# Kernel tuning notes

Hardware: AMD Instinct MI355X
Metric: run time of the kernel (lower is better)

The kernel has to match this reference:

```python
import jax, jax.numpy as jnp
import numpy as np

HIST_SIZE = 200
DIM = 64
HIDDEN = 32
NEG_INF = -2.0**32 + 1.0  # matches tf padding constant


def setup_inputs() -> dict:
    key = jax.random.key(0)
    k1, k2, k3, k4, k5 = jax.random.split(key, 5)
    B = 4096
    cand = jax.random.normal(k1, (B, DIM), dtype=jnp.float32)
    hist = jax.random.normal(k2, (B, HIST_SIZE, DIM), dtype=jnp.float32)
    hisLens = jax.random.randint(k3, (B,), 0, HIST_SIZE, dtype=jnp.int32)
    # Glorot-normal-ish params
    attW1 = jax.random.normal(k4, (4 * DIM, HIDDEN), dtype=jnp.float32) * (2.0 / (4 * DIM + HIDDEN)) ** 0.5
    attB1 = jnp.zeros((HIDDEN,), dtype=jnp.float32)
    attW2 = jax.random.normal(k5, (HIDDEN, 1), dtype=jnp.float32) * (2.0 / (HIDDEN + 1)) ** 0.5
    attB2 = jnp.zeros((1,), dtype=jnp.float32)
    return {"candidate_embedding": cand, "hist_embeddings": hist, "hisLens": hisLens,
            "attW1": attW1, "attB1": attB1, "attW2": attW2, "attB2": attB2}


def reference(candidate_embedding, hist_embeddings, hisLens, attW1, attB1, attW2, attB2):
    # candidate: [B, d] -> broadcast over hist steps [B, S, d]
    cand = candidate_embedding[:, None, :]
    # per-step feature concat: [cand, hist, cand*hist, cand-hist] -> [B, S, 4d]
    z3 = jnp.concatenate([
        jnp.broadcast_to(cand, hist_embeddings.shape),
        hist_embeddings,
        cand * hist_embeddings,
        cand - hist_embeddings,
    ], axis=-1)
    # tiny 2-layer MLP scorer -> [B, S]
    h = jax.nn.relu(jnp.einsum('bsf,fh->bsh', z3, attW1) + attB1)
    scores = (jnp.einsum('bsh,ho->bso', h, attW2) + attB2)[..., 0]
    # sequence mask then scale (same order as original), softmax over hist dim
    mask = jnp.arange(HIST_SIZE)[None, :] < hisLens[:, None]
    scores = jnp.where(mask, scores, NEG_INF) / (DIM ** 0.5)
    w = jax.nn.softmax(scores, axis=-1)  # [B, S]
    # weighted sum of history embeddings -> [B, d]
    return jnp.einsum('bs,bsd->bd', w, hist_embeddings)
```

## Files before the change

### kernel.cpp

```cpp
#include <hip/hip_runtime.h>
#include <math.h>

#define HS    200
#define DIMV  64
#define HID   32
#define NTH   256
#define NBPB  4

typedef __attribute__((ext_vector_type(8))) short short8;
typedef __attribute__((ext_vector_type(4))) float f32x4;
typedef __bf16 bf2_t __attribute__((ext_vector_type(2)));
typedef float  f2_t  __attribute__((ext_vector_type(2)));

__device__ __forceinline__ unsigned cvt2(float x, float y) {
    f2_t f = {x, y};
    bf2_t bv = __builtin_convertvector(f, bf2_t);
    union { bf2_t b; unsigned u; } un;
    un.b = bv;
    return un.u;
}
__device__ __forceinline__ float blo(unsigned u) { return __uint_as_float(u << 16); }
__device__ __forceinline__ float bhi(unsigned u) { return __uint_as_float(u & 0xFFFF0000u); }

template<int CTRL>
__device__ __forceinline__ float dpp_add(float x) {
    int y = __builtin_amdgcn_update_dpp(0, __float_as_int(x), CTRL, 0xF, 0xF, true);
    return x + __int_as_float(y);
}
#define ROR1  0x121
#define ROR2  0x122
#define ROR4  0x124
#define ROR8  0x128
#define QXOR1 0xB1
#define QXOR2 0x4E
#define HMIRR 0x141
__device__ __forceinline__ float swz_xor16(float x) {
    return __int_as_float(__builtin_amdgcn_ds_swizzle(__float_as_int(x), 0x401F));
}
__device__ __forceinline__ float rfl(float x) {
    return __int_as_float(__builtin_amdgcn_readfirstlane(__float_as_int(x)));
}


__global__ __launch_bounds__(NTH, 4) void din_attn_kernel(
    const float* __restrict__ cand,
    const float* __restrict__ hist,
    const int*   __restrict__ lens,
    const float* __restrict__ W1,
    const float* __restrict__ B1,
    const float* __restrict__ W2,
    const float* __restrict__ B2,
    float* __restrict__ out)
{
    __shared__ __align__(16) unsigned short s_Mt[NBPB][HID * 64];
    __shared__ float s_c[NBPB][HID];

    const int tid  = threadIdx.x;
    const int lane = tid & 63, wid = tid >> 6;
    const int b0   = blockIdx.x * NBPB;

    {
        const int h = tid & 31, fg = tid >> 5;
        float wbd[8], wcc[8];
        #pragma unroll
        for (int ff = 0; ff < 8; ++ff) {
            int f = fg * 8 + ff;
            wbd[ff] = W1[(DIMV + f) * HID + h] - W1[(3 * DIMV + f) * HID + h];
            wcc[ff] = W1[(2 * DIMV + f) * HID + h];
        }
        #pragma unroll
        for (int k = 0; k < NBPB; ++k) {
            const float* cb = cand + (size_t)(b0 + k) * DIMV + fg * 8;
            float4 cA = *(const float4*)cb;
            float4 cB = *(const float4*)(cb + 4);
            float cf[8] = {cA.x, cA.y, cA.z, cA.w, cB.x, cB.y, cB.z, cB.w};
            float m[8];
            #pragma unroll
            for (int ff = 0; ff < 8; ++ff) m[ff] = fmaf(cf[ff], wcc[ff], wbd[ff]);
            uint4 mw = make_uint4(cvt2(m[0], m[1]), cvt2(m[2], m[3]),
                                  cvt2(m[4], m[5]), cvt2(m[6], m[7]));
            *(uint4*)&s_Mt[k][h * 64 + (fg ^ (h & 7)) * 8] = mw;
        }
        const int hc = tid >> 3, fgc = tid & 7;
        float wad[8];
        #pragma unroll
        for (int ff = 0; ff < 8; ++ff) {
            int f = fgc * 8 + ff;
            wad[ff] = W1[f * HID + hc] + W1[(3 * DIMV + f) * HID + hc];
        }
        float b1 = B1[hc];
        #pragma unroll
        for (int k = 0; k < NBPB; ++k) {
            const float* cb = cand + (size_t)(b0 + k) * DIMV + fgc * 8;
            float4 cA = *(const float4*)cb;
            float4 cB = *(const float4*)(cb + 4);
            float p = cA.x * wad[0] + cA.y * wad[1] + cA.z * wad[2] + cA.w * wad[3]
                    + cB.x * wad[4] + cB.y * wad[5] + cB.z * wad[6] + cB.w * wad[7];
            p = dpp_add<QXOR1>(p);
            p = dpp_add<QXOR2>(p);
            p = dpp_add<HMIRR>(p);
            if ((tid & 7) == 0) s_c[k][hc] = p + b1;
        }
    }
    __syncthreads();

    const int b    = b0 + wid;
    const int len  = lens[b];
    const bool uni = (len == 0);
    const int nrow = uni ? HS : len;
    const int nt   = (nrow + 15) >> 4;
    const int lc   = lane & 15, lg = lane >> 4;
    const float* hb = hist + (size_t)b * (HS * DIMV);

    short8 b00 = *(const short8*)&s_Mt[wid][lc * 64        + ((lg)     ^ (lc & 7)) * 8];
    short8 b01 = *(const short8*)&s_Mt[wid][lc * 64        + ((4 + lg) ^ (lc & 7)) * 8];
    short8 b10 = *(const short8*)&s_Mt[wid][(16 + lc) * 64 + ((lg)     ^ (lc & 7)) * 8];
    short8 b11 = *(const short8*)&s_Mt[wid][(16 + lc) * 64 + ((4 + lg) ^ (lc & 7)) * 8];
    const float c0  = s_c[wid][lc],        c1  = s_c[wid][16 + lc];
    const float w20 = W2[lc] * 0.125f,     w21 = W2[16 + lc] * 0.125f;

    float m_run = -3.0e38f, l_acc = 0.f;
    float o0[8] = {0.f, 0.f, 0.f, 0.f, 0.f, 0.f, 0.f, 0.f};
    float o1[8] = {0.f, 0.f, 0.f, 0.f, 0.f, 0.f, 0.f, 0.f};

    auto ISSUE = [&](int rt, float4& X0, float4& X1, float4& X2, float4& X3) {
        int i = rt * 16 + lc;
        if (i > nrow - 1) i = nrow - 1;
        const float* ap = hb + i * 64 + lg * 8;
        X0 = *(const float4*)ap;
        X1 = *(const float4*)(ap + 4);
        X2 = *(const float4*)(ap + 32);
        X3 = *(const float4*)(ap + 36);
    };
    auto COMP = [&](int rt, const float4& X0, const float4& X1,
                            const float4& X2, const float4& X3) {
        union { uint4 u; short8 s8; } u0, u1;
        u0.u = make_uint4(cvt2(X0.x, X0.y), cvt2(X0.z, X0.w),
                          cvt2(X1.x, X1.y), cvt2(X1.z, X1.w));
        u1.u = make_uint4(cvt2(X2.x, X2.y), cvt2(X2.z, X2.w),
                          cvt2(X3.x, X3.y), cvt2(X3.z, X3.w));

        f32x4 acc0 = {c0, c0, c0, c0};
        acc0 = __builtin_amdgcn_mfma_f32_16x16x32_bf16(u0.s8, b00, acc0, 0, 0, 0);
        acc0 = __builtin_amdgcn_mfma_f32_16x16x32_bf16(u1.s8, b01, acc0, 0, 0, 0);
        f32x4 acc1 = {c1, c1, c1, c1};
        acc1 = __builtin_amdgcn_mfma_f32_16x16x32_bf16(u0.s8, b10, acc1, 0, 0, 0);
        acc1 = __builtin_amdgcn_mfma_f32_16x16x32_bf16(u1.s8, b11, acc1, 0, 0, 0);

        float p[4];
        #pragma unroll
        for (int r = 0; r < 4; ++r)
            p[r] = fmaxf(acc0[r], 0.f) * w20 + fmaxf(acc1[r], 0.f) * w21;
        #pragma unroll
        for (int r = 0; r < 4; ++r) {
            p[r] = dpp_add<ROR1>(p[r]);
            p[r] = dpp_add<ROR2>(p[r]);
            p[r] = dpp_add<ROR4>(p[r]);
            p[r] = dpp_add<ROR8>(p[r]);
        }
        #pragma unroll
        for (int r = 0; r < 4; ++r) {
            int row = rt * 16 + lg * 4 + r;
            p[r] = (row < nrow) ? (uni ? 0.f : p[r]) : -4.0e9f;
        }
        float tmax = fmaxf(fmaxf(p[0], p[1]), fmaxf(p[2], p[3]));
        tmax = fmaxf(tmax, swz_xor16(tmax));
        tmax = fmaxf(tmax, __shfl_xor(tmax, 32));
        tmax = rfl(tmax);
        if (tmax > m_run + 8.f) {
            float sf = __expf(m_run - tmax);
            #pragma unroll
            for (int j = 0; j < 8; ++j) { o0[j] *= sf; o1[j] *= sf; }
            l_acc *= sf;
            m_run = tmax;
        }
        float e[4];
        #pragma unroll
        for (int r = 0; r < 4; ++r) e[r] = __expf(p[r] - m_run);
        l_acc += (e[0] + e[1]) + (e[2] + e[3]);

        float t0 = (lc & 1) ? e[1] : e[0];
        float t1 = (lc & 1) ? e[3] : e[2];
        float es = (lc & 2) ? t1 : t0;
        int   src = (((lc & 3) | ((lc >> 2) << 4)) << 2);
        float wrow = __int_as_float(
            __builtin_amdgcn_ds_bpermute(src, __float_as_int(es)));

        o0[0] = fmaf(wrow, blo(u0.u.x), o0[0]); o0[1] = fmaf(wrow, bhi(u0.u.x), o0[1]);
        o0[2] = fmaf(wrow, blo(u0.u.y), o0[2]); o0[3] = fmaf(wrow, bhi(u0.u.y), o0[3]);
        o0[4] = fmaf(wrow, blo(u0.u.z), o0[4]); o0[5] = fmaf(wrow, bhi(u0.u.z), o0[5]);
        o0[6] = fmaf(wrow, blo(u0.u.w), o0[6]); o0[7] = fmaf(wrow, bhi(u0.u.w), o0[7]);
        o1[0] = fmaf(wrow, blo(u1.u.x), o1[0]); o1[1] = fmaf(wrow, bhi(u1.u.x), o1[1]);
        o1[2] = fmaf(wrow, blo(u1.u.y), o1[2]); o1[3] = fmaf(wrow, bhi(u1.u.y), o1[3]);
        o1[4] = fmaf(wrow, blo(u1.u.z), o1[4]); o1[5] = fmaf(wrow, bhi(u1.u.z), o1[5]);
        o1[6] = fmaf(wrow, blo(u1.u.w), o1[6]); o1[7] = fmaf(wrow, bhi(u1.u.w), o1[7]);
    };

    float4 F10, F11, F12, F13, F20, F21, F22, F23;
    ISSUE(0, F10, F11, F12, F13);
    ISSUE(1, F20, F21, F22, F23);
    for (int rt = 0; rt < nt; rt += 2) {
        {
            float4 X0 = F10, X1 = F11, X2 = F12, X3 = F13;
            ISSUE(rt + 2, F10, F11, F12, F13);
            COMP(rt, X0, X1, X2, X3);
        }
        if (rt + 1 < nt) {
            float4 X0 = F20, X1 = F21, X2 = F22, X3 = F23;
            ISSUE(rt + 3, F20, F21, F22, F23);
            COMP(rt + 1, X0, X1, X2, X3);
        }
    }

    l_acc += swz_xor16(l_acc);
    l_acc += __shfl_xor(l_acc, 32);
    const float inv = 1.0f / l_acc;
    #pragma unroll
    for (int j = 0; j < 8; ++j) {
        float x = o0[j];
        x = dpp_add<ROR1>(x); x = dpp_add<ROR2>(x);
        x = dpp_add<ROR4>(x); x = dpp_add<ROR8>(x);
        o0[j] = x * inv;
        float y = o1[j];
        y = dpp_add<ROR1>(y); y = dpp_add<ROR2>(y);
        y = dpp_add<ROR4>(y); y = dpp_add<ROR8>(y);
        o1[j] = y * inv;
    }
    if (lc == 0) {
        float* op = out + (size_t)b * DIMV + lg * 8;
        *(float4*)op        = make_float4(o0[0], o0[1], o0[2], o0[3]);
        *(float4*)(op + 4)  = make_float4(o0[4], o0[5], o0[6], o0[7]);
        *(float4*)(op + 32) = make_float4(o1[0], o1[1], o1[2], o1[3]);
        *(float4*)(op + 36) = make_float4(o1[4], o1[5], o1[6], o1[7]);
    }
}

extern "C" void kernel_launch(void* const* d_in, const int* in_sizes, int n_in,
                              void* d_out, int out_size, void* d_ws, size_t ws_size,
                              hipStream_t stream) {
    const float* cand = (const float*)d_in[0];
    const float* hist = (const float*)d_in[1];
    const int*   lens = (const int*)d_in[2];
    const float* W1   = (const float*)d_in[3];
    const float* B1   = (const float*)d_in[4];
    const float* W2   = (const float*)d_in[5];
    const float* B2   = (const float*)d_in[6];
    float* out = (float*)d_out;

    const int B = in_sizes[0] / DIMV;
    const int GRID = B / NBPB;
    din_attn_kernel<<<GRID, NTH, 0, stream>>>(cand, hist, lens, W1, B1, W2, B2, out);
}
```

Baseline: 32.81 us.

## Stage history tiles through LDS with coalesced row loads and double buffering

Global loads of history rows now read contiguous 16-float chunks per lane (four rows per quarter-wave), giving fully coalesced 256-byte row accesses. The values are converted to bf16 and written to a swizzled per-wave LDS tile, then read back in MFMA operand layout. A two-slot LDS ping-pong replaces the previous two-deep register prefetch. This trades extra LDS writes and reads, plus a shallower prefetch (one tile ahead instead of two), for better global access coalescing. No explicit wave barrier is needed because each wave uses its own tile.

```diff
diff --git a/kernel.cpp b/kernel.cpp
--- a/kernel.cpp
+++ b/kernel.cpp
@@ -53,6 +53,7 @@
     float* __restrict__ out)
 {
     __shared__ __align__(16) unsigned short s_Mt[NBPB][HID * 64];
+    __shared__ __align__(16) unsigned short s_tl[NBPB][2][16 * 64];
     __shared__ float s_c[NBPB][HID];
 
     const int tid  = threadIdx.x;
@@ -111,6 +112,8 @@
     const int nt   = (nrow + 15) >> 4;
     const int lc   = lane & 15, lg = lane >> 4;
     const float* hb = hist + (size_t)b * (HS * DIMV);
+    unsigned short* tl0 = s_tl[wid][0];
+    unsigned short* tl1 = s_tl[wid][1];
 
     short8 b00 = *(const short8*)&s_Mt[wid][lc * 64        + ((lg)     ^ (lc & 7)) * 8];
     short8 b01 = *(const short8*)&s_Mt[wid][lc * 64        + ((4 + lg) ^ (lc & 7)) * 8];
@@ -123,22 +126,35 @@
     float o0[8] = {0.f, 0.f, 0.f, 0.f, 0.f, 0.f, 0.f, 0.f};
     float o1[8] = {0.f, 0.f, 0.f, 0.f, 0.f, 0.f, 0.f, 0.f};
 
+    const int qrow = lane >> 4;
+    const int fch  = lane & 15;
+    const int wg   = fch >> 1, whalf = fch & 1;
+
     auto ISSUE = [&](int rt, float4& X0, float4& X1, float4& X2, float4& X3) {
-        int i = rt * 16 + lc;
-        if (i > nrow - 1) i = nrow - 1;
-        const float* ap = hb + i * 64 + lg * 8;
-        X0 = *(const float4*)ap;
-        X1 = *(const float4*)(ap + 4);
-        X2 = *(const float4*)(ap + 32);
-        X3 = *(const float4*)(ap + 36);
+        int r0 = rt * 16 + qrow;      if (r0 > nrow - 1) r0 = nrow - 1;
+        int r1 = rt * 16 + 4 + qrow;  if (r1 > nrow - 1) r1 = nrow - 1;
+        int r2 = rt * 16 + 8 + qrow;  if (r2 > nrow - 1) r2 = nrow - 1;
+        int r3 = rt * 16 + 12 + qrow; if (r3 > nrow - 1) r3 = nrow - 1;
+        X0 = *(const float4*)(hb + r0 * 64 + fch * 4);
+        X1 = *(const float4*)(hb + r1 * 64 + fch * 4);
+        X2 = *(const float4*)(hb + r2 * 64 + fch * 4);
+        X3 = *(const float4*)(hb + r3 * 64 + fch * 4);
     };
-    auto COMP = [&](int rt, const float4& X0, const float4& X1,
-                            const float4& X2, const float4& X3) {
+    auto CVTWRITE = [&](unsigned short* tl, const float4& X0, const float4& X1,
+                                            const float4& X2, const float4& X3) {
+        int rl0 = qrow,     g0 = wg ^ (rl0 & 7);
+        int rl1 = 4 + qrow, g1 = wg ^ (rl1 & 7);
+        int rl2 = 8 + qrow, g2 = wg ^ (rl2 & 7);
+        int rl3 = 12 + qrow, g3 = wg ^ (rl3 & 7);
+        *(uint2*)&tl[rl0 * 64 + g0 * 8 + whalf * 4] = make_uint2(cvt2(X0.x, X0.y), cvt2(X0.z, X0.w));
+        *(uint2*)&tl[rl1 * 64 + g1 * 8 + whalf * 4] = make_uint2(cvt2(X1.x, X1.y), cvt2(X1.z, X1.w));
+        *(uint2*)&tl[rl2 * 64 + g2 * 8 + whalf * 4] = make_uint2(cvt2(X2.x, X2.y), cvt2(X2.z, X2.w));
+        *(uint2*)&tl[rl3 * 64 + g3 * 8 + whalf * 4] = make_uint2(cvt2(X3.x, X3.y), cvt2(X3.z, X3.w));
+    };
+    auto COMP = [&](int rt, const unsigned short* tl) {
         union { uint4 u; short8 s8; } u0, u1;
-        u0.u = make_uint4(cvt2(X0.x, X0.y), cvt2(X0.z, X0.w),
-                          cvt2(X1.x, X1.y), cvt2(X1.z, X1.w));
-        u1.u = make_uint4(cvt2(X2.x, X2.y), cvt2(X2.z, X2.w),
-                          cvt2(X3.x, X3.y), cvt2(X3.z, X3.w));
+        u0.s8 = *(const short8*)&tl[lc * 64 + ((lg)     ^ (lc & 7)) * 8];
+        u1.s8 = *(const short8*)&tl[lc * 64 + ((4 + lg) ^ (lc & 7)) * 8];
 
         f32x4 acc0 = {c0, c0, c0, c0};
         acc0 = __builtin_amdgcn_mfma_f32_16x16x32_bf16(u0.s8, b00, acc0, 0, 0, 0);
@@ -196,20 +212,13 @@
         o1[6] = fmaf(wrow, blo(u1.u.w), o1[6]); o1[7] = fmaf(wrow, bhi(u1.u.w), o1[7]);
     };
 
-    float4 F10, F11, F12, F13, F20, F21, F22, F23;
-    ISSUE(0, F10, F11, F12, F13);
-    ISSUE(1, F20, F21, F22, F23);
-    for (int rt = 0; rt < nt; rt += 2) {
-        {
-            float4 X0 = F10, X1 = F11, X2 = F12, X3 = F13;
-            ISSUE(rt + 2, F10, F11, F12, F13);
-            COMP(rt, X0, X1, X2, X3);
-        }
-        if (rt + 1 < nt) {
-            float4 X0 = F20, X1 = F21, X2 = F22, X3 = F23;
-            ISSUE(rt + 3, F20, F21, F22, F23);
-            COMP(rt + 1, X0, X1, X2, X3);
-        }
+    float4 F0, F1, F2, F3;
+    ISSUE(0, F0, F1, F2, F3);
+    CVTWRITE(tl0, F0, F1, F2, F3);
+    for (int rt = 0; rt < nt; ++rt) {
+        if (rt + 1 < nt) ISSUE(rt + 1, F0, F1, F2, F3);
+        COMP(rt, (rt & 1) ? tl1 : tl0);
+        if (rt + 1 < nt) CVTWRITE((rt & 1) ? tl0 : tl1, F0, F1, F2, F3);
     }
 
     l_acc += swz_xor16(l_acc);
```

Result: faster. 32.01 us (-2.4%).
